# Kernel tuning notes

Measured on AMD Instinct MI355X. Metric: run time of the kernel, lower is better.

Reference implementation:

```python
import jax, jax.numpy as jnp
import numpy as np

HIDDEN = 2880
NUM_HEADS = 64
NUM_KV_HEADS = 8
HEAD_DIM = 64
ROPE_THETA = 150000.0
WINDOW = 128  # sliding window size (attend to last WINDOW tokens incl. current)
SCALE = HEAD_DIM ** -0.5
Q_SIZE = NUM_HEADS * HEAD_DIM          # 4096
KV_SIZE = NUM_KV_HEADS * HEAD_DIM      # 512


def _rope_neox(x, positions):
    # x: [T, n_heads, HEAD_DIM]; neox-style rotary over the full head dim
    half = HEAD_DIM // 2
    inv_freq = 1.0 / (ROPE_THETA ** (jnp.arange(half, dtype=jnp.float32) / half))
    freqs = positions.astype(jnp.float32)[:, None] * inv_freq[None, :]  # [T, half]
    cos = jnp.cos(freqs)[:, None, :]
    sin = jnp.sin(freqs)[:, None, :]
    x1, x2 = x[..., :half], x[..., half:]
    return jnp.concatenate([x1 * cos - x2 * sin, x2 * cos + x1 * sin], axis=-1)


def setup_inputs() -> dict:
    key = jax.random.key(0)
    k1, k2, k3, k4 = jax.random.split(key, 4)
    T = 2048
    hidden_states = jax.random.normal(k1, (T, HIDDEN), dtype=jnp.float32)
    positions = jnp.arange(T, dtype=jnp.int32)
    w_qkv = jax.random.normal(k2, (HIDDEN, Q_SIZE + 2 * KV_SIZE), dtype=jnp.float32) * (HIDDEN ** -0.5)
    w_o = jax.random.normal(k3, (Q_SIZE, HIDDEN), dtype=jnp.float32) * (Q_SIZE ** -0.5)
    sinks = jax.random.normal(k4, (NUM_HEADS,), dtype=jnp.float32)
    return {"positions": positions, "hidden_states": hidden_states,
            "w_qkv": w_qkv, "w_o": w_o, "sinks": sinks}


def reference(positions, hidden_states, w_qkv, w_o, sinks):
    T = hidden_states.shape[0]
    qkv = hidden_states @ w_qkv  # [T, 5120]
    q = qkv[:, :Q_SIZE].reshape(T, NUM_HEADS, HEAD_DIM)
    k = qkv[:, Q_SIZE:Q_SIZE + KV_SIZE].reshape(T, NUM_KV_HEADS, HEAD_DIM)
    v = qkv[:, Q_SIZE + KV_SIZE:].reshape(T, NUM_KV_HEADS, HEAD_DIM)

    q = _rope_neox(q, positions)
    k = _rope_neox(k, positions)

    # GQA: each group of NUM_HEADS//NUM_KV_HEADS query heads shares one kv head
    rep = NUM_HEADS // NUM_KV_HEADS
    k = jnp.repeat(k, rep, axis=1)  # [T, NUM_HEADS, HEAD_DIM]
    v = jnp.repeat(v, rep, axis=1)

    scores = jnp.einsum('qhd,khd->hqk', q, k) * SCALE  # [H, T, T]
    pos_q = positions[:, None]
    pos_k = positions[None, :]
    mask = (pos_k <= pos_q) & (pos_q - pos_k < WINDOW)  # causal + sliding window
    neg = jnp.finfo(scores.dtype).min
    scores = jnp.where(mask[None, :, :], scores, neg)

    # softmax with per-head learned sink logit included in the denominator
    m = jnp.maximum(scores.max(axis=-1), sinks[:, None])      # [H, T]
    e = jnp.exp(scores - m[..., None])                        # [H, T, T]
    denom = e.sum(axis=-1) + jnp.exp(sinks[:, None] - m)      # [H, T]
    probs = e / denom[..., None]

    attn = jnp.einsum('hqk,khd->qhd', probs, v).reshape(T, Q_SIZE)
    return attn @ w_o  # [T, HIDDEN]
```

## Files before the change

kernel.cpp:

```cpp
#include <hip/hip_runtime.h>
#include <hip/hip_bf16.h>

#define T_SEQ   2048
#define HIDDEN  2880
#define NQ      64
#define NKV     8
#define HD      64
#define QSIZE   4096
#define KVSIZE  512
#define QKV_N   5120
#define WINDOW  128
#define SCALE_F 0.125f
#define ROPE_L2 0.53733241958f

typedef unsigned short u16;
typedef __attribute__((ext_vector_type(8))) short short8;
typedef __attribute__((ext_vector_type(4))) float f32x4;

__device__ __forceinline__ u16 f2bf(float f) {
  __hip_bfloat16 b = __float2bfloat16(f);
  u16 u; __builtin_memcpy(&u, &b, 2); return u;
}

__device__ __forceinline__ void gload16(const u16* g, u16* l) {
  __builtin_amdgcn_global_load_lds(
      (const __attribute__((address_space(1))) void*)g,
      (__attribute__((address_space(3))) void*)l, 16, 0, 0);
}

#define ZERO_BLKS 1440
#define CAST_BLKS 5760
#define TQ_BX 80
#define TQ_BLKS (80 * 45)
#define TO_BX 45
#define TO_BLKS (45 * 64)
#define PREP_BLKS (ZERO_BLKS + CAST_BLKS + TQ_BLKS + TO_BLKS)

__global__ void prep_kernel(const float* __restrict__ hidden,
                            const float* __restrict__ w_qkv,
                            const float* __restrict__ w_o,
                            u16* __restrict__ Xb, u16* __restrict__ Wqt,
                            u16* __restrict__ Wot, float* __restrict__ dout) {
  __shared__ float tile[64][65];
  const int b = blockIdx.x, tid = threadIdx.x;
  if (b < ZERO_BLKS) {
    float4 z = {0.f, 0.f, 0.f, 0.f};
    ((float4*)dout)[(size_t)b * 256 + tid] = z;
    return;
  }
  if (b < ZERO_BLKS + CAST_BLKS) {
    size_t i = (size_t)(b - ZERO_BLKS) * 256 + tid;
    float4 v = ((const float4*)hidden)[i];
    ushort4 o;
    o.x = f2bf(v.x); o.y = f2bf(v.y); o.z = f2bf(v.z); o.w = f2bf(v.w);
    ((ushort4*)Xb)[i] = o;
    return;
  }
  const float* in; u16* out; int R, C, bx, by;
  if (b < ZERO_BLKS + CAST_BLKS + TQ_BLKS) {
    int bb = b - ZERO_BLKS - CAST_BLKS; bx = bb % TQ_BX; by = bb / TQ_BX;
    in = w_qkv; out = Wqt; R = HIDDEN; C = QKV_N;
  } else {
    int bb = b - ZERO_BLKS - CAST_BLKS - TQ_BLKS; bx = bb % TO_BX; by = bb / TO_BX;
    in = w_o; out = Wot; R = QSIZE; C = HIDDEN;
  }
  const int r0 = by * 64, c0 = bx * 64;
  const int tx = tid & 15, ty = tid >> 4;
#pragma unroll
  for (int i = 0; i < 4; ++i) {
    float4 v = *(const float4*)(in + (size_t)(r0 + ty + 16 * i) * C + c0 + tx * 4);
    tile[tx * 4 + 0][ty + 16 * i] = v.x;
    tile[tx * 4 + 1][ty + 16 * i] = v.y;
    tile[tx * 4 + 2][ty + 16 * i] = v.z;
    tile[tx * 4 + 3][ty + 16 * i] = v.w;
  }
  __syncthreads();
  const int rr8 = (tid & 7) * 8, cc0 = tid >> 3;
#pragma unroll
  for (int p = 0; p < 2; ++p) {
    int cc = cc0 + 32 * p;
    short8 o;
#pragma unroll
    for (int j = 0; j < 8; ++j) o[j] = (short)f2bf(tile[cc][rr8 + j]);
    *(short8*)(out + (size_t)(c0 + cc) * R + r0 + rr8) = o;
  }
}

template <int MODE>
__global__ __launch_bounds__(256)
void gemm_bt_kernel(const u16* __restrict__ A, const u16* __restrict__ B,
                    float* __restrict__ Cout, const int* __restrict__ positions,
                    u16* __restrict__ qb, u16* __restrict__ kb,
                    u16* __restrict__ vb, int Kstride, int NKT, int Ksplit,
                    int Bvalid, int Nout, int ldc, int NX, int NYC, int NY) {
  __shared__ __align__(16) u16 As[128 * 64];
  __shared__ __align__(16) u16 Bs[128 * 64];
  const int bb = blockIdx.x;
  const int xcd = bb & 7, bi = bb >> 3;
  const int ny = xcd * NYC + (bi % NYC);
  const int mx = bi / NYC;
  if (ny >= NY || mx >= NX) return;
  const int m0 = mx * 128, n0 = ny * 128;
  const int k0 = blockIdx.y * Ksplit;

  const int tid = threadIdx.x;
  const int lane = tid & 63, wave = tid >> 6;
  const int quad = lane >> 4, l16 = lane & 15;
  const int wm = wave >> 1, wn = wave & 1;

  const u16* Aptr[4]; const u16* Bptr[4]; u16* Alds[4]; u16* Blds[4];
#pragma unroll
  for (int it = 0; it < 4; ++it) {
    int c = it * 256 + tid;
    int r = c >> 3;
    int lcol = ((c & 7) ^ (r & 7)) * 8;
    Aptr[it] = A + (size_t)(m0 + r) * Kstride + k0 + lcol;
    int br = n0 + r; br = br < Bvalid ? br : Bvalid - 1;
    Bptr[it] = B + (size_t)br * Kstride + k0 + lcol;
    Alds[it] = As + c * 8;
    Blds[it] = Bs + c * 8;
  }

  f32x4 acc[4][4] = {};
  const int sw0 = (quad ^ (l16 & 7)) * 8;

  for (int t = 0, kt = 0; t < NKT; ++t, kt += 64) {
#pragma unroll
    for (int it = 0; it < 4; ++it) gload16(Aptr[it] + kt, Alds[it]);
#pragma unroll
    for (int it = 0; it < 4; ++it) gload16(Bptr[it] + kt, Blds[it]);
    asm volatile("s_waitcnt vmcnt(0)" ::: "memory");
    __syncthreads();
#pragma unroll
    for (int kk = 0; kk < 2; ++kk) {
      const int swo = sw0 ^ (kk * 32);
      short8 af[4], bf[4];
#pragma unroll
      for (int i = 0; i < 4; ++i)
        af[i] = *(const short8*)(As + (wm * 64 + i * 16 + l16) * 64 + swo);
#pragma unroll
      for (int j = 0; j < 4; ++j)
        bf[j] = *(const short8*)(Bs + (wn * 64 + j * 16 + l16) * 64 + swo);
#pragma unroll
      for (int i = 0; i < 4; ++i)
#pragma unroll
        for (int j = 0; j < 4; ++j)
          acc[i][j] = __builtin_amdgcn_mfma_f32_16x16x32_bf16(af[i], bf[j], acc[i][j], 0, 0, 0);
    }
    __syncthreads();
  }

  if (MODE == 0) {
#pragma unroll
    for (int i = 0; i < 4; ++i) {
      const int row = m0 + wm * 64 + i * 16 + quad * 4;
#pragma unroll
      for (int j = 0; j < 4; ++j) {
        const int col = n0 + wn * 64 + j * 16 + l16;
        if (col < Nout)
#pragma unroll
          for (int r = 0; r < 4; ++r)
            unsafeAtomicAdd(&Cout[(size_t)(row + r) * ldc + col], acc[i][j][r]);
      }
    }
  } else {
    const int region = (n0 < QSIZE) ? 0 : (n0 < QSIZE + KVSIZE ? 1 : 2);
    if (region <= 1) {
      float invs[2];
#pragma unroll
      for (int j = 0; j < 2; ++j)
        invs[j] = exp2f(-(float)(j * 16 + l16) * ROPE_L2);
#pragma unroll
      for (int i = 0; i < 4; ++i) {
#pragma unroll
        for (int r = 0; r < 4; ++r) {
          const int row = m0 + wm * 64 + i * 16 + quad * 4 + r;
          const float pos = (float)positions[row];
#pragma unroll
          for (int j = 0; j < 2; ++j) {
            float s, c;
            sincosf(pos * invs[j], &s, &c);
            const float x1 = acc[i][j][r], x2 = acc[i][j + 2][r];
            const float o1 = x1 * c - x2 * s, o2 = x2 * c + x1 * s;
            const int col = n0 + wn * 64 + j * 16 + l16;
            if (region == 0) {
              qb[(size_t)row * QSIZE + col] = f2bf(o1);
              qb[(size_t)row * QSIZE + col + 32] = f2bf(o2);
            } else {
              kb[(size_t)row * KVSIZE + col - QSIZE] = f2bf(o1);
              kb[(size_t)row * KVSIZE + col - QSIZE + 32] = f2bf(o2);
            }
          }
        }
      }
    } else {
#pragma unroll
      for (int i = 0; i < 4; ++i) {
        const int row = m0 + wm * 64 + i * 16 + quad * 4;
#pragma unroll
        for (int j = 0; j < 4; ++j) {
          const int col = n0 + wn * 64 + j * 16 + l16 - (QSIZE + KVSIZE);
#pragma unroll
          for (int r = 0; r < 4; ++r)
            vb[(size_t)(row + r) * KVSIZE + col] = f2bf(acc[i][j][r]);
        }
      }
    }
  }
}

__global__ __launch_bounds__(256, 2)
void attn_kernel(const u16* __restrict__ qb, const u16* __restrict__ kb,
                 const u16* __restrict__ vb, const float* __restrict__ sinks,
                 u16* __restrict__ attnb) {
  __shared__ __align__(16) u16 Ks[160 * 72];
  __shared__ __align__(16) u16 Vt[64 * 164];
  __shared__ __align__(16) u16 Pb[4 * 16 * 164];
  const int qt = blockIdx.x, g = blockIdx.y;
  const int q0 = qt * 32, kstart = q0 - 128;
  const int tid = threadIdx.x;
  const int lane = tid & 63, wave = tid >> 6;
  const int quad = lane >> 4, l16 = lane & 15;

  for (int s = tid; s < 1280; s += 256) {
    int r = s >> 3, c8 = (s & 7) * 8;
    int tg = kstart + r; tg = tg < 0 ? 0 : tg;
    *(short8*)(Ks + r * 72 + c8) =
        *(const short8*)(kb + (size_t)tg * KVSIZE + g * HD + c8);
  }
  {
    const u16* vbase = vb + g * HD;
#pragma unroll
    for (int it = 0; it < 5; ++it) {
      int s = it * 256 + tid;
      int r = s >> 3, c8 = (s & 7) * 8;
      int tg = kstart + r; tg = tg < 0 ? 0 : tg;
      gload16(vbase + (size_t)tg * KVSIZE + c8, Pb + s * 8);
    }
  }
  asm volatile("s_waitcnt vmcnt(0)" ::: "memory");
  __syncthreads();

  short8 bk[10][2];
#pragma unroll
  for (int jf = 0; jf < 10; ++jf)
#pragma unroll
    for (int kk = 0; kk < 2; ++kk)
      bk[jf][kk] = *(const short8*)(Ks + (jf * 16 + l16) * 72 + kk * 32 + quad * 8);

  for (int s = tid; s < 1280; s += 256) {
    int k8 = s >> 6, d = s & 63;
    short8 tmp;
#pragma unroll
    for (int j = 0; j < 8; ++j) tmp[j] = (short)Pb[(k8 * 8 + j) * 64 + d];
    *(short8*)(Vt + d * 164 + k8 * 8) = tmp;
  }
  __syncthreads();

  const int strip = wave & 1, hb = wave >> 1;
  const int qrow0 = q0 + strip * 16;
  u16* Pw = Pb + wave * 16 * 164;
  for (int hh = 0; hh < 4; ++hh) {
    const int h = g * 8 + hb + hh * 2;
    short8 aq[2];
#pragma unroll
    for (int kk = 0; kk < 2; ++kk)
      aq[kk] = *(const short8*)(qb + (size_t)(qrow0 + l16) * QSIZE + h * HD + kk * 32 + quad * 8);
    f32x4 sc[10];
#pragma unroll
    for (int jf = 0; jf < 10; ++jf) {
      f32x4 c = {0.f, 0.f, 0.f, 0.f};
#pragma unroll
      for (int kk = 0; kk < 2; ++kk)
        c = __builtin_amdgcn_mfma_f32_16x16x32_bf16(aq[kk], bk[jf][kk], c, 0, 0, 0);
      sc[jf] = c;
    }

    const float sink = sinks[h];
    float pinv[4];
#pragma unroll
    for (int r = 0; r < 4; ++r) {
      const int qg = qrow0 + quad * 4 + r;
      float mx = -3.0e38f;
#pragma unroll
      for (int jf = 0; jf < 10; ++jf) {
        int kg = kstart + jf * 16 + l16;
        bool valid = (kg >= 0) && (kg <= qg) && (qg - kg < WINDOW);
        float sv = valid ? sc[jf][r] * SCALE_F : -3.0e38f;
        sc[jf][r] = sv;
        mx = fmaxf(mx, sv);
      }
#pragma unroll
      for (int d = 1; d < 16; d <<= 1) mx = fmaxf(mx, __shfl_xor(mx, d, 64));
      mx = fmaxf(mx, sink);
      float sum = 0.f;
#pragma unroll
      for (int jf = 0; jf < 10; ++jf) {
        float e = __expf(sc[jf][r] - mx);
        sc[jf][r] = e;
        sum += e;
      }
#pragma unroll
      for (int d = 1; d < 16; d <<= 1) sum += __shfl_xor(sum, d, 64);
      sum += __expf(sink - mx);
      pinv[r] = 1.0f / sum;
    }

#pragma unroll
    for (int jf = 0; jf < 10; ++jf)
#pragma unroll
      for (int r = 0; r < 4; ++r)
        Pw[(quad * 4 + r) * 164 + jf * 16 + l16] = f2bf(sc[jf][r] * pinv[r]);

    f32x4 o[4] = {};
#pragma unroll
    for (int kk = 0; kk < 5; ++kk) {
      short8 ap = *(const short8*)(Pw + l16 * 164 + kk * 32 + quad * 8);
#pragma unroll
      for (int jf = 0; jf < 4; ++jf) {
        short8 bv = *(const short8*)(Vt + (jf * 16 + l16) * 164 + kk * 32 + quad * 8);
        o[jf] = __builtin_amdgcn_mfma_f32_16x16x32_bf16(ap, bv, o[jf], 0, 0, 0);
      }
    }
#pragma unroll
    for (int jf = 0; jf < 4; ++jf)
#pragma unroll
      for (int r = 0; r < 4; ++r) {
        int qg = qrow0 + quad * 4 + r;
        attnb[(size_t)qg * QSIZE + h * HD + jf * 16 + l16] = f2bf(o[jf][r]);
      }
  }
}

extern "C" void kernel_launch(void* const* d_in, const int* in_sizes, int n_in,
                              void* d_out, int out_size, void* d_ws, size_t ws_size,
                              hipStream_t stream) {
  (void)in_sizes; (void)n_in; (void)out_size; (void)ws_size;
  const int*   positions = (const int*)d_in[0];
  const float* hidden    = (const float*)d_in[1];
  const float* w_qkv     = (const float*)d_in[2];
  const float* w_o       = (const float*)d_in[3];
  const float* sinks     = (const float*)d_in[4];

  char* p = (char*)d_ws;
  u16* Xb    = (u16*)p; p += (size_t)T_SEQ * HIDDEN * 2;
  u16* Wqt   = (u16*)p; p += (size_t)QKV_N * HIDDEN * 2;
  u16* Wot   = (u16*)p; p += (size_t)HIDDEN * QSIZE * 2;
  u16* qb    = (u16*)p; p += (size_t)T_SEQ * QSIZE * 2;
  u16* kb    = (u16*)p; p += (size_t)T_SEQ * KVSIZE * 2;
  u16* vb    = (u16*)p; p += (size_t)T_SEQ * KVSIZE * 2;
  u16* attnb = (u16*)p; p += (size_t)T_SEQ * QSIZE * 2;

  prep_kernel<<<PREP_BLKS, 256, 0, stream>>>(hidden, w_qkv, w_o, Xb, Wqt, Wot,
                                             (float*)d_out);
  gemm_bt_kernel<1><<<dim3(16 * 8 * 5, 1), 256, 0, stream>>>(
      Xb, Wqt, nullptr, positions, qb, kb, vb,
      HIDDEN, 45, 0, QKV_N, QKV_N, QKV_N, 16, 5, 40);
  attn_kernel<<<dim3(T_SEQ / 32, NKV), 256, 0, stream>>>(qb, kb, vb, sinks, attnb);
  gemm_bt_kernel<0><<<dim3(16 * 8 * 3, 2), 256, 0, stream>>>(
      attnb, Wot, (float*)d_out, nullptr, nullptr, nullptr, nullptr,
      QSIZE, 32, 2048, HIDDEN, HIDDEN, HIDDEN, 16, 3, 23);
}
```

Before: 366.7 us.

## Fold W_o transpose into QKV GEMM launch, shrink M tile, drop split-K atomics

Moves the w_o transpose/cast from the prep kernel into extra blocks of the QKV GEMM launch, so that work overlaps with GEMM blocks. GEMM tiles shrink from 128x128 to 64x128 to create more blocks. The output GEMM no longer splits K with atomic adds, so it writes results directly and the output zeroing pass is removed. Smaller tiles lower data reuse per block and reduce parallelism in K for the output GEMM.

```diff
diff --git a/kernel.cpp b/kernel.cpp
--- a/kernel.cpp
+++ b/kernel.cpp
@@ -28,47 +28,31 @@
       (__attribute__((address_space(3))) void*)l, 16, 0, 0);
 }
 
-#define ZERO_BLKS 1440
 #define CAST_BLKS 5760
 #define TQ_BX 80
 #define TQ_BLKS (80 * 45)
-#define TO_BX 45
-#define TO_BLKS (45 * 64)
-#define PREP_BLKS (ZERO_BLKS + CAST_BLKS + TQ_BLKS + TO_BLKS)
+#define PREP_BLKS (CAST_BLKS + TQ_BLKS)
 
 __global__ void prep_kernel(const float* __restrict__ hidden,
                             const float* __restrict__ w_qkv,
-                            const float* __restrict__ w_o,
-                            u16* __restrict__ Xb, u16* __restrict__ Wqt,
-                            u16* __restrict__ Wot, float* __restrict__ dout) {
+                            u16* __restrict__ Xb, u16* __restrict__ Wqt) {
   __shared__ float tile[64][65];
   const int b = blockIdx.x, tid = threadIdx.x;
-  if (b < ZERO_BLKS) {
-    float4 z = {0.f, 0.f, 0.f, 0.f};
-    ((float4*)dout)[(size_t)b * 256 + tid] = z;
-    return;
-  }
-  if (b < ZERO_BLKS + CAST_BLKS) {
-    size_t i = (size_t)(b - ZERO_BLKS) * 256 + tid;
+  if (b < CAST_BLKS) {
+    size_t i = (size_t)b * 256 + tid;
     float4 v = ((const float4*)hidden)[i];
     ushort4 o;
     o.x = f2bf(v.x); o.y = f2bf(v.y); o.z = f2bf(v.z); o.w = f2bf(v.w);
     ((ushort4*)Xb)[i] = o;
     return;
   }
-  const float* in; u16* out; int R, C, bx, by;
-  if (b < ZERO_BLKS + CAST_BLKS + TQ_BLKS) {
-    int bb = b - ZERO_BLKS - CAST_BLKS; bx = bb % TQ_BX; by = bb / TQ_BX;
-    in = w_qkv; out = Wqt; R = HIDDEN; C = QKV_N;
-  } else {
-    int bb = b - ZERO_BLKS - CAST_BLKS - TQ_BLKS; bx = bb % TO_BX; by = bb / TO_BX;
-    in = w_o; out = Wot; R = QSIZE; C = HIDDEN;
-  }
+  const int bb = b - CAST_BLKS;
+  const int bx = bb % TQ_BX, by = bb / TQ_BX;
   const int r0 = by * 64, c0 = bx * 64;
   const int tx = tid & 15, ty = tid >> 4;
 #pragma unroll
   for (int i = 0; i < 4; ++i) {
-    float4 v = *(const float4*)(in + (size_t)(r0 + ty + 16 * i) * C + c0 + tx * 4);
+    float4 v = *(const float4*)(w_qkv + (size_t)(r0 + ty + 16 * i) * QKV_N + c0 + tx * 4);
     tile[tx * 4 + 0][ty + 16 * i] = v.x;
     tile[tx * 4 + 1][ty + 16 * i] = v.y;
     tile[tx * 4 + 2][ty + 16 * i] = v.z;
@@ -82,7 +66,7 @@
     short8 o;
 #pragma unroll
     for (int j = 0; j < 8; ++j) o[j] = (short)f2bf(tile[cc][rr8 + j]);
-    *(short8*)(out + (size_t)(c0 + cc) * R + r0 + rr8) = o;
+    *(short8*)(Wqt + (size_t)(c0 + cc) * HIDDEN + r0 + rr8) = o;
   }
 }
 
@@ -91,42 +75,79 @@
 void gemm_bt_kernel(const u16* __restrict__ A, const u16* __restrict__ B,
                     float* __restrict__ Cout, const int* __restrict__ positions,
                     u16* __restrict__ qb, u16* __restrict__ kb,
-                    u16* __restrict__ vb, int Kstride, int NKT, int Ksplit,
-                    int Bvalid, int Nout, int ldc, int NX, int NYC, int NY) {
-  __shared__ __align__(16) u16 As[128 * 64];
-  __shared__ __align__(16) u16 Bs[128 * 64];
+                    u16* __restrict__ vb, const float* __restrict__ tin,
+                    u16* __restrict__ tout, int Kstride, int NKT,
+                    int Bvalid, int Nout, int ldc, int NX, int NYC, int NY,
+                    int GEMM_BLKS) {
+  __shared__ __align__(16) u16 smem[(64 + 128) * 64];
+  const int tid = threadIdx.x;
   const int bb = blockIdx.x;
+
+  if (MODE == 1 && bb >= GEMM_BLKS) {
+    float (*tile)[65] = (float (*)[65])smem;
+    const int bt = bb - GEMM_BLKS;
+    const int bx = bt % 45, by = bt / 45;
+    const int r0 = by * 64, c0 = bx * 64;
+    const int tx = tid & 15, ty = tid >> 4;
+#pragma unroll
+    for (int i = 0; i < 4; ++i) {
+      float4 v = *(const float4*)(tin + (size_t)(r0 + ty + 16 * i) * HIDDEN + c0 + tx * 4);
+      tile[tx * 4 + 0][ty + 16 * i] = v.x;
+      tile[tx * 4 + 1][ty + 16 * i] = v.y;
+      tile[tx * 4 + 2][ty + 16 * i] = v.z;
+      tile[tx * 4 + 3][ty + 16 * i] = v.w;
+    }
+    __syncthreads();
+    const int rr8 = (tid & 7) * 8, cc0 = tid >> 3;
+#pragma unroll
+    for (int p = 0; p < 2; ++p) {
+      int cc = cc0 + 32 * p;
+      short8 o;
+#pragma unroll
+      for (int j = 0; j < 8; ++j) o[j] = (short)f2bf(tile[cc][rr8 + j]);
+      *(short8*)(tout + (size_t)(c0 + cc) * QSIZE + r0 + rr8) = o;
+    }
+    return;
+  }
+
   const int xcd = bb & 7, bi = bb >> 3;
   const int ny = xcd * NYC + (bi % NYC);
   const int mx = bi / NYC;
   if (ny >= NY || mx >= NX) return;
-  const int m0 = mx * 128, n0 = ny * 128;
-  const int k0 = blockIdx.y * Ksplit;
-
-  const int tid = threadIdx.x;
+  const int m0 = mx * 64, n0 = ny * 128;
+
   const int lane = tid & 63, wave = tid >> 6;
   const int quad = lane >> 4, l16 = lane & 15;
   const int wm = wave >> 1, wn = wave & 1;
 
-  const u16* Aptr[4]; const u16* Bptr[4]; u16* Alds[4]; u16* Blds[4];
+  u16* As = smem;
+  u16* Bs = smem + 64 * 64;
+
+  const u16* Aptr[2]; const u16* Bptr[4]; u16* Alds[2]; u16* Blds[4];
+#pragma unroll
+  for (int it = 0; it < 2; ++it) {
+    int c = it * 256 + tid;
+    int r = c >> 3;
+    int lcol = ((c & 7) ^ (r & 7)) * 8;
+    Aptr[it] = A + (size_t)(m0 + r) * Kstride + lcol;
+    Alds[it] = As + c * 8;
+  }
 #pragma unroll
   for (int it = 0; it < 4; ++it) {
     int c = it * 256 + tid;
     int r = c >> 3;
     int lcol = ((c & 7) ^ (r & 7)) * 8;
-    Aptr[it] = A + (size_t)(m0 + r) * Kstride + k0 + lcol;
     int br = n0 + r; br = br < Bvalid ? br : Bvalid - 1;
-    Bptr[it] = B + (size_t)br * Kstride + k0 + lcol;
-    Alds[it] = As + c * 8;
+    Bptr[it] = B + (size_t)br * Kstride + lcol;
     Blds[it] = Bs + c * 8;
   }
 
-  f32x4 acc[4][4] = {};
+  f32x4 acc[2][4] = {};
   const int sw0 = (quad ^ (l16 & 7)) * 8;
 
   for (int t = 0, kt = 0; t < NKT; ++t, kt += 64) {
 #pragma unroll
-    for (int it = 0; it < 4; ++it) gload16(Aptr[it] + kt, Alds[it]);
+    for (int it = 0; it < 2; ++it) gload16(Aptr[it] + kt, Alds[it]);
 #pragma unroll
     for (int it = 0; it < 4; ++it) gload16(Bptr[it] + kt, Blds[it]);
     asm volatile("s_waitcnt vmcnt(0)" ::: "memory");
@@ -134,15 +155,15 @@
 #pragma unroll
     for (int kk = 0; kk < 2; ++kk) {
       const int swo = sw0 ^ (kk * 32);
-      short8 af[4], bf[4];
-#pragma unroll
-      for (int i = 0; i < 4; ++i)
-        af[i] = *(const short8*)(As + (wm * 64 + i * 16 + l16) * 64 + swo);
+      short8 af[2], bf[4];
+#pragma unroll
+      for (int i = 0; i < 2; ++i)
+        af[i] = *(const short8*)(As + (wm * 32 + i * 16 + l16) * 64 + swo);
 #pragma unroll
       for (int j = 0; j < 4; ++j)
         bf[j] = *(const short8*)(Bs + (wn * 64 + j * 16 + l16) * 64 + swo);
 #pragma unroll
-      for (int i = 0; i < 4; ++i)
+      for (int i = 0; i < 2; ++i)
 #pragma unroll
         for (int j = 0; j < 4; ++j)
           acc[i][j] = __builtin_amdgcn_mfma_f32_16x16x32_bf16(af[i], bf[j], acc[i][j], 0, 0, 0);
@@ -152,15 +173,15 @@
 
   if (MODE == 0) {
 #pragma unroll
-    for (int i = 0; i < 4; ++i) {
-      const int row = m0 + wm * 64 + i * 16 + quad * 4;
+    for (int i = 0; i < 2; ++i) {
+      const int row = m0 + wm * 32 + i * 16 + quad * 4;
 #pragma unroll
       for (int j = 0; j < 4; ++j) {
         const int col = n0 + wn * 64 + j * 16 + l16;
         if (col < Nout)
 #pragma unroll
           for (int r = 0; r < 4; ++r)
-            unsafeAtomicAdd(&Cout[(size_t)(row + r) * ldc + col], acc[i][j][r]);
+            Cout[(size_t)(row + r) * ldc + col] = acc[i][j][r];
       }
     }
   } else {
@@ -171,10 +192,10 @@
       for (int j = 0; j < 2; ++j)
         invs[j] = exp2f(-(float)(j * 16 + l16) * ROPE_L2);
 #pragma unroll
-      for (int i = 0; i < 4; ++i) {
+      for (int i = 0; i < 2; ++i) {
 #pragma unroll
         for (int r = 0; r < 4; ++r) {
-          const int row = m0 + wm * 64 + i * 16 + quad * 4 + r;
+          const int row = m0 + wm * 32 + i * 16 + quad * 4 + r;
           const float pos = (float)positions[row];
 #pragma unroll
           for (int j = 0; j < 2; ++j) {
@@ -195,8 +216,8 @@
       }
     } else {
 #pragma unroll
-      for (int i = 0; i < 4; ++i) {
-        const int row = m0 + wm * 64 + i * 16 + quad * 4;
+      for (int i = 0; i < 2; ++i) {
+        const int row = m0 + wm * 32 + i * 16 + quad * 4;
 #pragma unroll
         for (int j = 0; j < 4; ++j) {
           const int col = n0 + wn * 64 + j * 16 + l16 - (QSIZE + KVSIZE);
@@ -351,13 +372,12 @@
   u16* vb    = (u16*)p; p += (size_t)T_SEQ * KVSIZE * 2;
   u16* attnb = (u16*)p; p += (size_t)T_SEQ * QSIZE * 2;
 
-  prep_kernel<<<PREP_BLKS, 256, 0, stream>>>(hidden, w_qkv, w_o, Xb, Wqt, Wot,
-                                             (float*)d_out);
-  gemm_bt_kernel<1><<<dim3(16 * 8 * 5, 1), 256, 0, stream>>>(
-      Xb, Wqt, nullptr, positions, qb, kb, vb,
-      HIDDEN, 45, 0, QKV_N, QKV_N, QKV_N, 16, 5, 40);
+  prep_kernel<<<PREP_BLKS, 256, 0, stream>>>(hidden, w_qkv, Xb, Wqt);
+  gemm_bt_kernel<1><<<32 * 8 * 5 + 45 * 64, 256, 0, stream>>>(
+      Xb, Wqt, nullptr, positions, qb, kb, vb, w_o, Wot,
+      HIDDEN, 45, QKV_N, QKV_N, QKV_N, 32, 5, 40, 32 * 8 * 5);
   attn_kernel<<<dim3(T_SEQ / 32, NKV), 256, 0, stream>>>(qb, kb, vb, sinks, attnb);
-  gemm_bt_kernel<0><<<dim3(16 * 8 * 3, 2), 256, 0, stream>>>(
+  gemm_bt_kernel<0><<<32 * 8 * 3, 256, 0, stream>>>(
       attnb, Wot, (float*)d_out, nullptr, nullptr, nullptr, nullptr,
-      QSIZE, 32, 2048, HIDDEN, HIDDEN, HIDDEN, 16, 3, 23);
-}
+      nullptr, nullptr, QSIZE, 64, HIDDEN, HIDDEN, HIDDEN, 32, 3, 23, 32 * 8 * 3);
+}
```

After: 318.9 us. 13.0% less time.
